# Kernel optimization log

Measured on AMD Instinct MI355X. Metric: run time of the kernel, lower is better.

## Reference

```python
import jax, jax.numpy as jnp
import numpy as np

B, S, E, H, ROT, MAXP = 2, 1024, 2048, 16, 64, 2048
HD = E // H
EPS = 1e-12  # torch F.normalize default eps


def _sinusoidal_positions(num_pos, dim):
    # GPT-J create_sinusoidal_positions: concat(sin, cos) along feature dim
    inv_freq = 1.0 / (10000.0 ** (np.arange(0, dim, 2, dtype=np.float32) / dim))
    sinusoid = np.einsum("i,j->ij", np.arange(num_pos, dtype=np.float32), inv_freq)
    return jnp.asarray(np.concatenate([np.sin(sinusoid), np.cos(sinusoid)], axis=-1))


def _rotate_every_two(x):
    x1 = x[..., ::2]
    x2 = x[..., 1::2]
    return jnp.stack((-x2, x1), axis=-1).reshape(x.shape)


def _apply_rotary(t, sin, cos):
    # t: [B,S,H,rot]; sin/cos: [B,S,rot/2] -> repeat_interleave(2) -> [B,S,1,rot]
    sin = jnp.repeat(sin, 2, axis=-1)[:, :, None, :]
    cos = jnp.repeat(cos, 2, axis=-1)[:, :, None, :]
    return t * cos + _rotate_every_two(t) * sin


def setup_inputs() -> dict:
    key = jax.random.key(0)
    ks = jax.random.split(key, 5)
    hidden_states = jax.random.normal(ks[0], (B, S, E), dtype=jnp.float32)
    w_q = jax.random.normal(ks[1], (E, E), dtype=jnp.float32) * 0.02
    w_k = jax.random.normal(ks[2], (E, E), dtype=jnp.float32) * 0.02
    w_v = jax.random.normal(ks[3], (E, E), dtype=jnp.float32) * 0.02
    w_o = jax.random.normal(ks[4], (E, E), dtype=jnp.float32) * 0.02
    norm_const = 0.5 * jnp.ones((1, H, 1, 1), dtype=jnp.float32)
    attention_mask = jnp.zeros((B, 1, 1, S), dtype=jnp.float32)  # 0 = attend (HF additive mask)
    position_ids = jnp.tile(jnp.arange(S, dtype=jnp.int32)[None, :], (B, 1))
    return {"hidden_states": hidden_states, "w_q": w_q, "w_k": w_k, "w_v": w_v,
            "w_o": w_o, "norm_const": norm_const, "attention_mask": attention_mask,
            "position_ids": position_ids}


def reference(hidden_states, w_q, w_k, w_v, w_o, norm_const, attention_mask, position_ids):
    b, s, e = hidden_states.shape
    # projections (nn.Linear, no bias): y = x @ W.T
    q = (hidden_states @ w_q.T).reshape(b, s, H, HD)  # rotary layout [B,S,H,hd]
    k = (hidden_states @ w_k.T).reshape(b, s, H, HD)
    v = (hidden_states @ w_v.T).reshape(b, s, H, HD).transpose(0, 2, 1, 3)  # [B,H,S,hd]

    embed = _sinusoidal_positions(MAXP, ROT)          # [MAXP, ROT]
    sincos = embed[position_ids]                      # [B,S,ROT]
    sin, cos = jnp.split(sincos, 2, axis=-1)          # each [B,S,ROT/2]

    # partial rotary on first ROT dims
    q = jnp.concatenate([_apply_rotary(q[..., :ROT], sin, cos), q[..., ROT:]], axis=-1)
    k = jnp.concatenate([_apply_rotary(k[..., :ROT], sin, cos), k[..., ROT:]], axis=-1)
    q = q.transpose(0, 2, 1, 3)  # [B,H,S,hd]
    k = k.transpose(0, 2, 1, 3)

    causal = jnp.tril(jnp.ones((s, s), dtype=bool))[None, None]   # [1,1,S,S]
    mask0 = (attention_mask == 0)                                  # [B,1,1,S] bool

    # value rescale: per-query count of visible keys ** sigmoid(norm_const), clamped >= 1
    counts = jnp.sum(causal & mask0, axis=-1, keepdims=True).astype(jnp.float32)  # [B,1,S,1]
    denom = jnp.maximum(counts ** jax.nn.sigmoid(norm_const), 1.0)                # [B,H,S,1]
    v = v / denom

    # L2-normalize q/k (torch F.normalize: x / max(||x||, eps))
    q = q / jnp.maximum(jnp.linalg.norm(q, axis=-1, keepdims=True), EPS)
    k = k / jnp.maximum(jnp.linalg.norm(k, axis=-1, keepdims=True), EPS)

    mask_t = jnp.swapaxes(mask0, -1, -2)  # [B,1,S,1]
    q = q * mask_t
    k = k * mask_t
    v = v * mask_t

    attn_weights = jnp.einsum("bhqd,bhkd->bhqk", q, k)     # cosine similarities
    attn_weights = jnp.where(causal, attn_weights, 0.0)
    attn_output = jnp.einsum("bhqk,bhkd->bhqd", attn_weights, v)

    attn_output = attn_output.transpose(0, 2, 1, 3).reshape(b, s, e)
    return attn_output @ w_o.T
```

## Files before the change

### kernel.cpp

```cpp
#include <hip/hip_runtime.h>
#include <math.h>

#define B 2
#define S 1024
#define E 2048
#define H 16
#define HD 128
#define ROT 64
#define EPSN 1e-12f

using half8 = __attribute__((ext_vector_type(8))) _Float16;
using half4 = __attribute__((ext_vector_type(4))) _Float16;
using half2 = __attribute__((ext_vector_type(2))) _Float16;
using f32x4 = __attribute__((ext_vector_type(4))) float;

__device__ __forceinline__ void gl_lds16(const void* g, void* l) {
    __builtin_amdgcn_global_load_lds(
        (const __attribute__((address_space(1))) unsigned int*)g,
        (__attribute__((address_space(3))) unsigned int*)l, 16, 0, 0);
}

#define BARX()  asm volatile("s_barrier" ::: "memory")
#define LGKM0() asm volatile("s_waitcnt lgkmcnt(0)" ::: "memory")
#define VMW(n)  asm volatile("s_waitcnt vmcnt(" #n ")" ::: "memory")

__global__ __launch_bounds__(256) void f2h5(const float* __restrict__ x0,
                                            const float* __restrict__ x1,
                                            const float* __restrict__ x2,
                                            const float* __restrict__ x3,
                                            const float* __restrict__ x4,
                                            _Float16* __restrict__ y0,
                                            _Float16* __restrict__ y1,
                                            _Float16* __restrict__ y2,
                                            _Float16* __restrict__ y3,
                                            _Float16* __restrict__ y4) {
    const float* xs[5] = {x0, x1, x2, x3, x4};
    _Float16*    ys[5] = {y0, y1, y2, y3, y4};
    const int t = blockIdx.y;
    const int i = blockIdx.x * 256 + threadIdx.x;
    float4 v = ((const float4*)xs[t])[i];
    half4 h;
    h[0] = (_Float16)v.x; h[1] = (_Float16)v.y;
    h[2] = (_Float16)v.z; h[3] = (_Float16)v.w;
    ((half4*)ys[t])[i] = h;
}

__global__ __launch_bounds__(512, 2) void gemm_qkv256(
        const _Float16* __restrict__ hs,
        const _Float16* __restrict__ wq,
        const _Float16* __restrict__ wk,
        const _Float16* __restrict__ wv,
        _Float16* __restrict__ qo,
        _Float16* __restrict__ ko,
        _Float16* __restrict__ vo) {
    __shared__ uint4 L[8][1024];

    const int lid = (int)blockIdx.x;
    const int swz = (lid & 7) * 24 + (lid >> 3);
    const int z   = swz >> 6;
    const int gm  = (swz & 63) >> 3;
    const int gn  = swz & 7;
    const _Float16* Wp = (z == 0) ? wq : (z == 1) ? wk : wv;
    _Float16*     Cout = (z == 0) ? qo : (z == 1) ? ko : vo;
    const int mBase = gm << 8;
    const int nBase = gn << 8;

    const int tid   = (int)threadIdx.x;
    const int lane  = tid & 63;
    const int w     = tid >> 6;
    const int l15   = lane & 15;
    const int lq    = lane >> 4;
    const int wm4   = (w >> 2) << 2;
    const int wn2   = (w & 3) << 1;
    const int wbase = tid & 448;

    f32x4 acc[2][2][4][2];
#pragma unroll
    for (int X = 0; X < 2; ++X)
#pragma unroll
        for (int Y = 0; Y < 2; ++Y)
#pragma unroll
            for (int mt = 0; mt < 4; ++mt)
#pragma unroll
                for (int nt = 0; nt < 2; ++nt)
                    acc[X][Y][mt][nt] = (f32x4){0.f, 0.f, 0.f, 0.f};

    half8 af[4][2], wf[2][2];

    auto stage = [&](int slot, const _Float16* src, int rowBase, int hf, int kt) {
#pragma unroll
        for (int j = 0; j < 2; ++j) {
            const int c  = (j << 9) + tid;
            const int rb = c >> 7;
            const int q  = (c >> 4) & 7;
            const int r  = c & 15;
            gl_lds16(&src[(size_t)(rowBase + hf * 128 + rb * 16 + r) * E +
                          kt * 64 + q * 8],
                     &L[slot][(j << 9) + wbase]);
        }
    };
    auto ldsA = [&](int db, int X) {
#pragma unroll
        for (int mt = 0; mt < 4; ++mt)
#pragma unroll
            for (int ks = 0; ks < 2; ++ks)
                af[mt][ks] = *(const half8*)&L[db * 2 + X]
                    [(wm4 + mt) * 128 + (ks * 4 + lq) * 16 + l15];
    };
    auto ldsB = [&](int db, int Y) {
#pragma unroll
        for (int nt = 0; nt < 2; ++nt)
#pragma unroll
            for (int ks = 0; ks < 2; ++ks)
                wf[nt][ks] = *(const half8*)&L[4 + db * 2 + Y]
                    [(wn2 + nt) * 128 + (ks * 4 + lq) * 16 + l15];
    };
    auto mma = [&](int X, int Y) {
        __builtin_amdgcn_s_setprio(1);
#pragma unroll
        for (int mt = 0; mt < 4; ++mt)
#pragma unroll
            for (int nt = 0; nt < 2; ++nt)
#pragma unroll
                for (int ks = 0; ks < 2; ++ks)
                    acc[X][Y][mt][nt] = __builtin_amdgcn_mfma_f32_16x16x32_f16(
                        af[mt][ks], wf[nt][ks], acc[X][Y][mt][nt], 0, 0, 0);
        __builtin_amdgcn_s_setprio(0);
    };

    stage(0, hs, mBase, 0, 0);
    stage(4, Wp, nBase, 0, 0);
    stage(1, hs, mBase, 1, 0);
    stage(5, Wp, nBase, 1, 0);
    stage(2, hs, mBase, 0, 1);
    stage(7, Wp, nBase, 1, 1);
    stage(3, hs, mBase, 1, 1);
    VMW(6);
    BARX();

    for (int j = 0; j < 16; ++j) {
        const int tB  = 2 * j + 1;
        const int tN0 = 2 * j + 2;
        const int tN1 = 2 * j + 3;
        const bool more = (j < 15);

        ldsA(0, 0); ldsB(0, 0);
        stage(6, Wp, nBase, 0, tB);
        BARX(); LGKM0();
        mma(0, 0);
        BARX();

        ldsB(0, 1);
        if (more) stage(0, hs, mBase, 0, tN0);
        BARX(); LGKM0();
        mma(0, 1);
        BARX();

        ldsA(0, 1);
        if (more) stage(5, Wp, nBase, 1, tN0);
        BARX(); LGKM0();
        mma(1, 1);
        BARX();

        ldsB(0, 0);
        if (more) { stage(1, hs, mBase, 1, tN0); VMW(4); }
        else      { VMW(0); }
        BARX(); LGKM0();
        mma(1, 0);
        BARX();

        ldsA(1, 0); ldsB(1, 0);
        if (more) stage(4, Wp, nBase, 0, tN0);
        BARX(); LGKM0();
        mma(0, 0);
        BARX();

        ldsB(1, 1);
        if (more) stage(2, hs, mBase, 0, tN1);
        BARX(); LGKM0();
        mma(0, 1);
        BARX();

        ldsA(1, 1);
        if (more) stage(7, Wp, nBase, 1, tN1);
        BARX(); LGKM0();
        mma(1, 1);
        BARX();

        ldsB(1, 0);
        if (more) stage(3, hs, mBase, 1, tN1);
        VMW(4);
        BARX(); LGKM0();
        mma(1, 0);
        BARX();
    }

#pragma unroll
    for (int X = 0; X < 2; ++X)
#pragma unroll
        for (int Y = 0; Y < 2; ++Y)
#pragma unroll
            for (int mt = 0; mt < 4; ++mt)
#pragma unroll
                for (int nt = 0; nt < 2; ++nt)
#pragma unroll
                    for (int r = 0; r < 4; ++r) {
                        int row = mBase + X * 128 + (w >> 2) * 64 + mt * 16 + lq * 4 + r;
                        int col = nBase + Y * 128 + (w & 3) * 32 + nt * 16 + l15;
                        int b = row >> 10, s = row & (S - 1);
                        int h = col >> 7,  d = col & (HD - 1);
                        Cout[(((size_t)b * H + h) * S + s) * HD + d] =
                            (_Float16)acc[X][Y][mt][nt][r];
                    }
}

__global__ __launch_bounds__(256) void gemm_out(const _Float16* __restrict__ A,
                                                const _Float16* __restrict__ Wp,
                                                float* __restrict__ C) {
    __shared__ uint4 As_l[2][512];
    __shared__ uint4 Ws_l[2][512];
    const int lid = (int)blockIdx.x;
    const int swz = (lid & 7) * 32 + (lid >> 3);
    const int gm  = swz >> 4;
    const int gn  = swz & 15;
    const int tid  = threadIdx.x;
    const int lane = tid & 63;
    const int w    = tid >> 6;
    const int wm   = (w >> 1) * 64;
    const int wn   = (w & 1) * 64;
    const int l15  = lane & 15;
    const int lq   = lane >> 4;
    const int r16  = lane & 15;
    const int kq4  = lane >> 4;
    const int mBase = gm * 128;
    const int nBase = gn * 128;

    f32x4 acc[4][4];
#pragma unroll
    for (int mt = 0; mt < 4; ++mt)
#pragma unroll
        for (int nt = 0; nt < 4; ++nt)
            acc[mt][nt] = (f32x4){0.f, 0.f, 0.f, 0.f};

    auto stage = [&](int bf, int k0) {
#pragma unroll
        for (int i = 0; i < 2; ++i) {
            int rb = w * 2 + i;
            gl_lds16(&A[(size_t)(mBase + rb * 16 + r16) * E + k0 + kq4 * 8],
                     &As_l[bf][rb * 64]);
            gl_lds16(&Wp[(size_t)(nBase + rb * 16 + r16) * E + k0 + kq4 * 8],
                     &Ws_l[bf][rb * 64]);
        }
    };

    stage(0, 0);
    const int nIter = E / 32;
    for (int it = 0; it < nIter; ++it) {
        __syncthreads();
        if (it + 1 < nIter) stage((it + 1) & 1, (it + 1) * 32);

        const int cur = it & 1;
        half8 af[4], wfr[4];
#pragma unroll
        for (int t = 0; t < 4; ++t) {
            int rbA = (wm >> 4) + t;
            int rbW = (wn >> 4) + t;
            af[t]  = *(const half8*)&As_l[cur][rbA * 64 + lq * 16 + l15];
            wfr[t] = *(const half8*)&Ws_l[cur][rbW * 64 + lq * 16 + l15];
        }
#pragma unroll
        for (int mt = 0; mt < 4; ++mt)
#pragma unroll
            for (int nt = 0; nt < 4; ++nt)
                acc[mt][nt] = __builtin_amdgcn_mfma_f32_16x16x32_f16(
                    af[mt], wfr[nt], acc[mt][nt], 0, 0, 0);
    }

#pragma unroll
    for (int mt = 0; mt < 4; ++mt)
#pragma unroll
        for (int nt = 0; nt < 4; ++nt)
#pragma unroll
            for (int r = 0; r < 4; ++r) {
                int row = mBase + wm + mt * 16 + lq * 4 + r;
                int col = nBase + wn + nt * 16 + l15;
                C[(size_t)row * E + col] = acc[mt][nt][r];
            }
}

__global__ __launch_bounds__(256) void rotary_norm(_Float16* __restrict__ qh,
                                                   _Float16* __restrict__ kh,
                                                   const float* __restrict__ am,
                                                   const int* __restrict__ pos) {
    const int wave = threadIdx.x >> 6;
    const int lane = threadIdx.x & 63;
    const int item = blockIdx.x * 4 + wave;
    const int b = item / (H * S);
    const int h = (item / S) % H;
    const int s = item % S;

    const float p = (float)pos[b * S + s];
    float co = 1.f, si = 0.f;
    if (lane < 32) {
        float ang = p * expf(-0.28782313662425574f * (float)lane);
        sincosf(ang, &si, &co);
    }
    const float valid = (am[b * S + s] == 0.f) ? 1.f : 0.f;
    const size_t base = ((size_t)(b * H + h) * S + s) * HD;

    _Float16* bufs[2] = {qh, kh};
#pragma unroll
    for (int a = 0; a < 2; ++a) {
        _Float16* ptr = bufs[a];
        half2 xin = *(const half2*)&ptr[base + 2 * lane];
        float x0 = (float)xin[0], x1 = (float)xin[1];
        float y0, y1;
        if (lane < 32) {
            y0 = x0 * co - x1 * si;
            y1 = x1 * co + x0 * si;
        } else {
            y0 = x0;
            y1 = x1;
        }
        float ss = y0 * y0 + y1 * y1;
#pragma unroll
        for (int off = 32; off > 0; off >>= 1)
            ss += __shfl_xor(ss, off);
        float scale = valid / fmaxf(sqrtf(ss), EPSN);
        half2 xo;
        xo[0] = (_Float16)(y0 * scale);
        xo[1] = (_Float16)(y1 * scale);
        *(half2*)&ptr[base + 2 * lane] = xo;
    }
}

__global__ __launch_bounds__(256) void vprep(const _Float16* __restrict__ v,
                                             _Float16* __restrict__ vt,
                                             const float* __restrict__ am,
                                             const float* __restrict__ nc) {
    __shared__ _Float16 T[HD][72];
    __shared__ float sscale[64];
    const int bh = blockIdx.y;
    const int b = bh >> 4, h = bh & 15;
    const int s0 = blockIdx.x * 64;
    const int tid = threadIdx.x;

    if (tid < 64) {
        const int lane = tid;
        float basec = 0.f;
        for (int j0 = 0; j0 < s0; j0 += 64) {
            float z = (am[b * S + j0 + lane] == 0.f) ? 1.f : 0.f;
#pragma unroll
            for (int off = 32; off > 0; off >>= 1)
                z += __shfl_xor(z, off);
            basec += z;
        }
        float zown = (am[b * S + s0 + lane] == 0.f) ? 1.f : 0.f;
        float sc = zown;
#pragma unroll
        for (int off = 1; off < 64; off <<= 1) {
            float u = __shfl_up(sc, off);
            if (lane >= off) sc += u;
        }
        float cntv = basec + sc;
        float sig = 1.f / (1.f + expf(-nc[h]));
        float denom = fmaxf(powf(cntv, sig), 1.f);
        sscale[lane] = zown / denom;
    }
    __syncthreads();

#pragma unroll
    for (int j = 0; j < 4; ++j) {
        int f = tid + j * 256;
        int s = f >> 4, c8 = f & 15;
        half8 x = *(const half8*)&v[((size_t)bh * S + s0 + s) * HD + c8 * 8];
        float sc = sscale[s];
#pragma unroll
        for (int i = 0; i < 8; ++i)
            T[c8 * 8 + i][s] = (_Float16)((float)x[i] * sc);
    }
    __syncthreads();

#pragma unroll
    for (int j = 0; j < 4; ++j) {
        int f = tid + j * 256;
        int d = f >> 3, c8 = f & 7;
        *(uint4*)&vt[((size_t)bh * HD + d) * S + s0 + c8 * 8] =
            *(const uint4*)&T[d][c8 * 8];
    }
}

__global__ __launch_bounds__(256) void attn_mfma(const _Float16* __restrict__ qh,
                                                 const _Float16* __restrict__ kh,
                                                 const _Float16* __restrict__ vt,
                                                 _Float16* __restrict__ o) {
    __shared__ _Float16 Ks[64][136];
    __shared__ _Float16 Vs[HD][72];
    __shared__ _Float16 Ps[64][72];

    const int qt = (int)gridDim.x - 1 - (int)blockIdx.x;
    const int bh = blockIdx.y;
    const int b = bh >> 4, h = bh & 15;
    const int tid = threadIdx.x;
    const int lane = tid & 63;
    const int w = tid >> 6;
    const int l15 = lane & 15;
    const int lq = lane >> 4;
    const int qBase = qt * 64;
    const size_t sd_base = (size_t)bh * S * HD;

    half8 qf[4];
#pragma unroll
    for (int ks = 0; ks < 4; ++ks)
        qf[ks] = *(const half8*)&qh[sd_base + (size_t)(qBase + w * 16 + l15) * HD +
                                    ks * 32 + lq * 8];

    f32x4 oacc[8];
#pragma unroll
    for (int dt = 0; dt < 8; ++dt)
        oacc[dt] = (f32x4){0.f, 0.f, 0.f, 0.f};

    const int nkc = qt + 1;
    uint4 pk[4], pv[4];
#pragma unroll
    for (int j = 0; j < 4; ++j) {
        int f = tid + j * 256;
        int rK = f >> 4, c8K = f & 15;
        int rV = f >> 3, c8V = f & 7;
        pk[j] = *(const uint4*)&kh[sd_base + (size_t)rK * HD + c8K * 8];
        pv[j] = *(const uint4*)&vt[sd_base + (size_t)rV * S + c8V * 8];
    }

    for (int kc = 0; kc < nkc; ++kc) {
        __syncthreads();
#pragma unroll
        for (int j = 0; j < 4; ++j) {
            int f = tid + j * 256;
            int rK = f >> 4, c8K = f & 15;
            int rV = f >> 3, c8V = f & 7;
            *(uint4*)&Ks[rK][c8K * 8] = pk[j];
            *(uint4*)&Vs[rV][c8V * 8] = pv[j];
        }
        __syncthreads();

        if (kc + 1 < nkc) {
            const int kB = (kc + 1) * 64;
#pragma unroll
            for (int j = 0; j < 4; ++j) {
                int f = tid + j * 256;
                int rK = f >> 4, c8K = f & 15;
                int rV = f >> 3, c8V = f & 7;
                pk[j] = *(const uint4*)&kh[sd_base + (size_t)(kB + rK) * HD + c8K * 8];
                pv[j] = *(const uint4*)&vt[sd_base + (size_t)rV * S + kB + c8V * 8];
            }
        }

        const int kBase = kc * 64;
        f32x4 sacc[4];
#pragma unroll
        for (int nt = 0; nt < 4; ++nt)
            sacc[nt] = (f32x4){0.f, 0.f, 0.f, 0.f};
#pragma unroll
        for (int nt = 0; nt < 4; ++nt)
#pragma unroll
            for (int ks = 0; ks < 4; ++ks) {
                half8 kf = *(const half8*)&Ks[nt * 16 + l15][ks * 32 + lq * 8];
                sacc[nt] = __builtin_amdgcn_mfma_f32_16x16x32_f16(qf[ks], kf,
                                                                  sacc[nt], 0, 0, 0);
            }

#pragma unroll
        for (int nt = 0; nt < 4; ++nt)
#pragma unroll
            for (int r = 0; r < 4; ++r) {
                int qg = qBase + w * 16 + lq * 4 + r;
                int kg = kBase + nt * 16 + l15;
                float sv = (kg <= qg) ? sacc[nt][r] : 0.f;
                Ps[w * 16 + lq * 4 + r][nt * 16 + l15] = (_Float16)sv;
            }

        half8 pf[2];
        pf[0] = *(const half8*)&Ps[w * 16 + l15][lq * 8];
        pf[1] = *(const half8*)&Ps[w * 16 + l15][32 + lq * 8];
#pragma unroll
        for (int dt = 0; dt < 8; ++dt)
#pragma unroll
            for (int ks = 0; ks < 2; ++ks) {
                half8 vf = *(const half8*)&Vs[dt * 16 + l15][ks * 32 + lq * 8];
                oacc[dt] = __builtin_amdgcn_mfma_f32_16x16x32_f16(pf[ks], vf,
                                                                  oacc[dt], 0, 0, 0);
            }
    }

#pragma unroll
    for (int dt = 0; dt < 8; ++dt)
#pragma unroll
        for (int r = 0; r < 4; ++r) {
            size_t off = (size_t)(b * S + qBase + w * 16 + lq * 4 + r) * E +
                         h * HD + dt * 16 + l15;
            o[off] = (_Float16)oacc[dt][r];
        }
}

extern "C" void kernel_launch(void* const* d_in, const int* in_sizes, int n_in,
                              void* d_out, int out_size, void* d_ws, size_t ws_size,
                              hipStream_t stream) {
    (void)in_sizes; (void)n_in; (void)out_size; (void)ws_size;
    const float* hs = (const float*)d_in[0];
    const float* wq = (const float*)d_in[1];
    const float* wk = (const float*)d_in[2];
    const float* wv = (const float*)d_in[3];
    const float* wo = (const float*)d_in[4];
    const float* nc = (const float*)d_in[5];
    const float* am = (const float*)d_in[6];
    const int*  pos = (const int*)d_in[7];
    float* out = (float*)d_out;

    const size_t act = (size_t)B * S * E;
    _Float16* hsb = (_Float16*)d_ws;
    _Float16* wqb = hsb + act;
    _Float16* wkb = wqb + act;
    _Float16* wvb = wkb + act;
    _Float16* wob = wvb + act;
    _Float16* qhh = wob + act;
    _Float16* khh = qhh + act;
    _Float16* vhh = khh + act;
    _Float16* vtt = vhh + act;
    _Float16* abb = vtt + act;

    f2h5<<<dim3((int)(act / 4 / 256), 5), 256, 0, stream>>>(
        hs, wq, wk, wv, wo, hsb, wqb, wkb, wvb, wob);

    gemm_qkv256<<<192, 512, 0, stream>>>(hsb, wqb, wkb, wvb, qhh, khh, vhh);

    rotary_norm<<<(B * H * S) / 4, 256, 0, stream>>>(qhh, khh, am, pos);
    vprep<<<dim3(S / 64, B * H), 256, 0, stream>>>(vhh, vtt, am, nc);

    attn_mfma<<<dim3(S / 64, B * H), 256, 0, stream>>>(qhh, khh, vtt, abb);

    gemm_out<<<256, 256, 0, stream>>>(abb, wob, out);
}
```

Before: 357.3 us.

## Replace quadratic causal attention with chunked linear attention using prefix K^T V states

The attention has no softmax, so causal attention can be computed as a linear recurrence. The new code forms per-chunk K^T V outer products in fp16, prefix-sums them across 16 chunks, and has each query tile combine Q times its prefix state with an intra-chunk masked local attention. This removes the serial loop over all earlier key chunks in the attention kernel. In exchange it adds a K transpose, two extra kernels, a 16 MB intermediate written and read in workspace aliased onto the freed weight buffers, and fp16 rounding of accumulated states.

```diff
diff --git a/kernel.cpp b/kernel.cpp
--- a/kernel.cpp
+++ b/kernel.cpp
@@ -335,7 +335,9 @@
 }
 
 __global__ __launch_bounds__(256) void vprep(const _Float16* __restrict__ v,
+                                             const _Float16* __restrict__ k,
                                              _Float16* __restrict__ vt,
+                                             _Float16* __restrict__ kt,
                                              const float* __restrict__ am,
                                              const float* __restrict__ nc) {
     __shared__ _Float16 T[HD][72];
@@ -380,7 +382,6 @@
             T[c8 * 8 + i][s] = (_Float16)((float)x[i] * sc);
     }
     __syncthreads();
-
 #pragma unroll
     for (int j = 0; j < 4; ++j) {
         int f = tid + j * 256;
@@ -388,17 +389,134 @@
         *(uint4*)&vt[((size_t)bh * HD + d) * S + s0 + c8 * 8] =
             *(const uint4*)&T[d][c8 * 8];
     }
-}
-
-__global__ __launch_bounds__(256) void attn_mfma(const _Float16* __restrict__ qh,
-                                                 const _Float16* __restrict__ kh,
-                                                 const _Float16* __restrict__ vt,
-                                                 _Float16* __restrict__ o) {
+
+    __syncthreads();
+#pragma unroll
+    for (int j = 0; j < 4; ++j) {
+        int f = tid + j * 256;
+        int s = f >> 4, c8 = f & 15;
+        half8 x = *(const half8*)&k[((size_t)bh * S + s0 + s) * HD + c8 * 8];
+#pragma unroll
+        for (int i = 0; i < 8; ++i)
+            T[c8 * 8 + i][s] = x[i];
+    }
+    __syncthreads();
+#pragma unroll
+    for (int j = 0; j < 4; ++j) {
+        int f = tid + j * 256;
+        int d = f >> 3, c8 = f & 7;
+        *(uint4*)&kt[((size_t)bh * HD + d) * S + s0 + c8 * 8] =
+            *(const uint4*)&T[d][c8 * 8];
+    }
+}
+
+__global__ __launch_bounds__(256) void kvouter(const _Float16* __restrict__ kt,
+                                               const _Float16* __restrict__ vt,
+                                               _Float16* __restrict__ ut) {
+    __shared__ __align__(16) _Float16 SB[2 * 128 * 72];
+    _Float16 (*Kt_s)[72] = (_Float16(*)[72])SB;
+    _Float16 (*Vt_s)[72] = (_Float16(*)[72])(SB + 128 * 72);
+    const int c  = blockIdx.x;
+    const int bh = blockIdx.y;
+    const int tid = threadIdx.x;
+    const int lane = tid & 63, w = tid >> 6;
+    const int l15 = lane & 15, lq = lane >> 4;
+    const size_t ds_b = (size_t)bh * HD * S + (size_t)c * 64;
+
+    uint4 pk[4], pv[4];
+#pragma unroll
+    for (int j = 0; j < 4; ++j) {
+        int f = tid + j * 256;
+        int d = f >> 3, c8 = f & 7;
+        pk[j] = *(const uint4*)&kt[ds_b + (size_t)d * S + c8 * 8];
+        pv[j] = *(const uint4*)&vt[ds_b + (size_t)d * S + c8 * 8];
+    }
+#pragma unroll
+    for (int j = 0; j < 4; ++j) {
+        int f = tid + j * 256;
+        int d = f >> 3, c8 = f & 7;
+        *(uint4*)&Kt_s[d][c8 * 8] = pk[j];
+        *(uint4*)&Vt_s[d][c8 * 8] = pv[j];
+    }
+    __syncthreads();
+
+    f32x4 acc[2][8];
+#pragma unroll
+    for (int mt = 0; mt < 2; ++mt)
+#pragma unroll
+        for (int nt = 0; nt < 8; ++nt)
+            acc[mt][nt] = (f32x4){0.f, 0.f, 0.f, 0.f};
+
+#pragma unroll
+    for (int ks = 0; ks < 2; ++ks) {
+        half8 af[2], wf[8];
+#pragma unroll
+        for (int mt = 0; mt < 2; ++mt)
+            af[mt] = *(const half8*)&Kt_s[(w * 2 + mt) * 16 + l15][ks * 32 + lq * 8];
+#pragma unroll
+        for (int nt = 0; nt < 8; ++nt)
+            wf[nt] = *(const half8*)&Vt_s[nt * 16 + l15][ks * 32 + lq * 8];
+#pragma unroll
+        for (int mt = 0; mt < 2; ++mt)
+#pragma unroll
+            for (int nt = 0; nt < 8; ++nt)
+                acc[mt][nt] = __builtin_amdgcn_mfma_f32_16x16x32_f16(
+                    af[mt], wf[nt], acc[mt][nt], 0, 0, 0);
+    }
+    __syncthreads();
+
+    _Float16* Mb = SB;
+#pragma unroll
+    for (int mt = 0; mt < 2; ++mt)
+#pragma unroll
+        for (int nt = 0; nt < 8; ++nt)
+#pragma unroll
+            for (int r = 0; r < 4; ++r) {
+                int dk = (w * 2 + mt) * 16 + lq * 4 + r;
+                int flat = nt * 2048 + (dk >> 5) * 512 +
+                           (l15 + ((dk >> 3) & 3) * 16) * 8 + (dk & 7);
+                Mb[flat] = (_Float16)acc[mt][nt][r];
+            }
+    __syncthreads();
+
+    const size_t ub = ((size_t)bh * 16 + c) << 14;
+#pragma unroll
+    for (int j = 0; j < 8; ++j) {
+        int f = tid + j * 256;
+        *(uint4*)&ut[ub + (size_t)f * 8] = *(const uint4*)&Mb[f * 8];
+    }
+}
+
+__global__ __launch_bounds__(256) void prefix16(_Float16* __restrict__ u) {
+    const int sl = blockIdx.x & 7;
+    const int bh = blockIdx.x >> 3;
+    const size_t base = (size_t)bh * 16 * 16384 + sl * 2048 + threadIdx.x * 8;
+    float acc[8] = {0.f, 0.f, 0.f, 0.f, 0.f, 0.f, 0.f, 0.f};
+    half8 nxt = *(const half8*)&u[base];
+#pragma unroll
+    for (int c = 0; c < 16; ++c) {
+        half8 cur = nxt;
+        if (c < 15) nxt = *(const half8*)&u[base + (size_t)(c + 1) * 16384];
+        half8 outv;
+#pragma unroll
+        for (int i = 0; i < 8; ++i) outv[i] = (_Float16)acc[i];
+        *(half8*)&u[base + (size_t)c * 16384] = outv;
+#pragma unroll
+        for (int i = 0; i < 8; ++i) acc[i] += (float)cur[i];
+    }
+}
+
+__global__ __launch_bounds__(256) void attn_local(const _Float16* __restrict__ qh,
+                                                  const _Float16* __restrict__ kh,
+                                                  const _Float16* __restrict__ vt,
+                                                  const _Float16* __restrict__ mt,
+                                                  _Float16* __restrict__ o) {
     __shared__ _Float16 Ks[64][136];
     __shared__ _Float16 Vs[HD][72];
     __shared__ _Float16 Ps[64][72];
-
-    const int qt = (int)gridDim.x - 1 - (int)blockIdx.x;
+    __shared__ uint4 Ms[2048];
+
+    const int qt = blockIdx.x;
     const int bh = blockIdx.y;
     const int b = bh >> 4, h = bh & 15;
     const int tid = threadIdx.x;
@@ -415,91 +533,93 @@
         qf[ks] = *(const half8*)&qh[sd_base + (size_t)(qBase + w * 16 + l15) * HD +
                                     ks * 32 + lq * 8];
 
+    const _Float16* mtc = mt + (((size_t)bh * 16 + qt) << 14);
+#pragma unroll
+    for (int rr = 0; rr < 8; ++rr)
+        gl_lds16(&mtc[(size_t)((rr * 4 + w) * 64 + lane) * 8],
+                 &Ms[(rr * 4 + w) * 64]);
+
+    uint4 pk[4], pv[4];
+#pragma unroll
+    for (int j = 0; j < 4; ++j) {
+        int f = tid + j * 256;
+        int rK = f >> 4, c8K = f & 15;
+        int rV = f >> 3, c8V = f & 7;
+        pk[j] = *(const uint4*)&kh[sd_base + (size_t)(qBase + rK) * HD + c8K * 8];
+        pv[j] = *(const uint4*)&vt[sd_base + (size_t)rV * S + qBase + c8V * 8];
+    }
+#pragma unroll
+    for (int j = 0; j < 4; ++j) {
+        int f = tid + j * 256;
+        int rK = f >> 4, c8K = f & 15;
+        int rV = f >> 3, c8V = f & 7;
+        *(uint4*)&Ks[rK][c8K * 8] = pk[j];
+        *(uint4*)&Vs[rV][c8V * 8] = pv[j];
+    }
+    __syncthreads();
+
+    f32x4 sacc[4];
+#pragma unroll
+    for (int nt = 0; nt < 4; ++nt)
+        sacc[nt] = (f32x4){0.f, 0.f, 0.f, 0.f};
+#pragma unroll
+    for (int nt = 0; nt < 4; ++nt)
+#pragma unroll
+        for (int ks = 0; ks < 4; ++ks) {
+            half8 kf = *(const half8*)&Ks[nt * 16 + l15][ks * 32 + lq * 8];
+            sacc[nt] = __builtin_amdgcn_mfma_f32_16x16x32_f16(qf[ks], kf,
+                                                              sacc[nt], 0, 0, 0);
+        }
+
+#pragma unroll
+    for (int nt = 0; nt < 4; ++nt)
+#pragma unroll
+        for (int r = 0; r < 4; ++r) {
+            int ql = w * 16 + lq * 4 + r;
+            int kl = nt * 16 + l15;
+            float sv = (kl <= ql) ? sacc[nt][r] : 0.f;
+            Ps[ql][kl] = (_Float16)sv;
+        }
+
     f32x4 oacc[8];
 #pragma unroll
     for (int dt = 0; dt < 8; ++dt)
         oacc[dt] = (f32x4){0.f, 0.f, 0.f, 0.f};
-
-    const int nkc = qt + 1;
-    uint4 pk[4], pv[4];
-#pragma unroll
-    for (int j = 0; j < 4; ++j) {
-        int f = tid + j * 256;
-        int rK = f >> 4, c8K = f & 15;
-        int rV = f >> 3, c8V = f & 7;
-        pk[j] = *(const uint4*)&kh[sd_base + (size_t)rK * HD + c8K * 8];
-        pv[j] = *(const uint4*)&vt[sd_base + (size_t)rV * S + c8V * 8];
-    }
-
-    for (int kc = 0; kc < nkc; ++kc) {
-        __syncthreads();
-#pragma unroll
-        for (int j = 0; j < 4; ++j) {
-            int f = tid + j * 256;
-            int rK = f >> 4, c8K = f & 15;
-            int rV = f >> 3, c8V = f & 7;
-            *(uint4*)&Ks[rK][c8K * 8] = pk[j];
-            *(uint4*)&Vs[rV][c8V * 8] = pv[j];
-        }
-        __syncthreads();
-
-        if (kc + 1 < nkc) {
-            const int kB = (kc + 1) * 64;
-#pragma unroll
-            for (int j = 0; j < 4; ++j) {
-                int f = tid + j * 256;
-                int rK = f >> 4, c8K = f & 15;
-                int rV = f >> 3, c8V = f & 7;
-                pk[j] = *(const uint4*)&kh[sd_base + (size_t)(kB + rK) * HD + c8K * 8];
-                pv[j] = *(const uint4*)&vt[sd_base + (size_t)rV * S + kB + c8V * 8];
-            }
-        }
-
-        const int kBase = kc * 64;
-        f32x4 sacc[4];
-#pragma unroll
-        for (int nt = 0; nt < 4; ++nt)
-            sacc[nt] = (f32x4){0.f, 0.f, 0.f, 0.f};
-#pragma unroll
-        for (int nt = 0; nt < 4; ++nt)
-#pragma unroll
-            for (int ks = 0; ks < 4; ++ks) {
-                half8 kf = *(const half8*)&Ks[nt * 16 + l15][ks * 32 + lq * 8];
-                sacc[nt] = __builtin_amdgcn_mfma_f32_16x16x32_f16(qf[ks], kf,
-                                                                  sacc[nt], 0, 0, 0);
-            }
-
-#pragma unroll
-        for (int nt = 0; nt < 4; ++nt)
-#pragma unroll
-            for (int r = 0; r < 4; ++r) {
-                int qg = qBase + w * 16 + lq * 4 + r;
-                int kg = kBase + nt * 16 + l15;
-                float sv = (kg <= qg) ? sacc[nt][r] : 0.f;
-                Ps[w * 16 + lq * 4 + r][nt * 16 + l15] = (_Float16)sv;
-            }
-
-        half8 pf[2];
-        pf[0] = *(const half8*)&Ps[w * 16 + l15][lq * 8];
-        pf[1] = *(const half8*)&Ps[w * 16 + l15][32 + lq * 8];
-#pragma unroll
-        for (int dt = 0; dt < 8; ++dt)
-#pragma unroll
-            for (int ks = 0; ks < 2; ++ks) {
-                half8 vf = *(const half8*)&Vs[dt * 16 + l15][ks * 32 + lq * 8];
-                oacc[dt] = __builtin_amdgcn_mfma_f32_16x16x32_f16(pf[ks], vf,
-                                                                  oacc[dt], 0, 0, 0);
-            }
-    }
-
 #pragma unroll
     for (int dt = 0; dt < 8; ++dt)
 #pragma unroll
-        for (int r = 0; r < 4; ++r) {
-            size_t off = (size_t)(b * S + qBase + w * 16 + lq * 4 + r) * E +
-                         h * HD + dt * 16 + l15;
-            o[off] = (_Float16)oacc[dt][r];
-        }
+        for (int km = 0; km < 4; ++km) {
+            half8 mf = *(const half8*)&Ms[(dt * 4 + km) * 64 + lane];
+            oacc[dt] = __builtin_amdgcn_mfma_f32_16x16x32_f16(qf[km], mf,
+                                                              oacc[dt], 0, 0, 0);
+        }
+    __syncthreads();
+
+    half8 pf[2];
+    pf[0] = *(const half8*)&Ps[w * 16 + l15][lq * 8];
+    pf[1] = *(const half8*)&Ps[w * 16 + l15][32 + lq * 8];
+#pragma unroll
+    for (int dt = 0; dt < 8; ++dt)
+#pragma unroll
+        for (int ks = 0; ks < 2; ++ks) {
+            half8 vf = *(const half8*)&Vs[dt * 16 + l15][ks * 32 + lq * 8];
+            oacc[dt] = __builtin_amdgcn_mfma_f32_16x16x32_f16(pf[ks], vf,
+                                                              oacc[dt], 0, 0, 0);
+        }
+
+#pragma unroll
+    for (int dt = 0; dt < 8; ++dt)
+#pragma unroll
+        for (int r = 0; r < 4; ++r)
+            Ks[w * 16 + lq * 4 + r][dt * 16 + l15] = (_Float16)oacc[dt][r];
+    __syncthreads();
+#pragma unroll
+    for (int j = 0; j < 4; ++j) {
+        int f = tid + j * 256;
+        int ql = f >> 4, c8 = f & 15;
+        *(uint4*)&o[(size_t)(b * S + qBase + ql) * E + h * HD + c8 * 8] =
+            *(const uint4*)&Ks[ql][c8 * 8];
+    }
 }
 
 extern "C" void kernel_launch(void* const* d_in, const int* in_sizes, int n_in,
@@ -527,6 +647,8 @@
     _Float16* vhh = khh + act;
     _Float16* vtt = vhh + act;
     _Float16* abb = vtt + act;
+    _Float16* ktt = hsb;
+    _Float16* utm = wqb;
 
     f2h5<<<dim3((int)(act / 4 / 256), 5), 256, 0, stream>>>(
         hs, wq, wk, wv, wo, hsb, wqb, wkb, wvb, wob);
@@ -534,9 +656,11 @@
     gemm_qkv256<<<192, 512, 0, stream>>>(hsb, wqb, wkb, wvb, qhh, khh, vhh);
 
     rotary_norm<<<(B * H * S) / 4, 256, 0, stream>>>(qhh, khh, am, pos);
-    vprep<<<dim3(S / 64, B * H), 256, 0, stream>>>(vhh, vtt, am, nc);
-
-    attn_mfma<<<dim3(S / 64, B * H), 256, 0, stream>>>(qhh, khh, vtt, abb);
+    vprep<<<dim3(S / 64, B * H), 256, 0, stream>>>(vhh, khh, vtt, ktt, am, nc);
+
+    kvouter<<<dim3(16, B * H), 256, 0, stream>>>(ktt, vtt, utm);
+    prefix16<<<B * H * 8, 256, 0, stream>>>(utm);
+    attn_local<<<dim3(16, B * H), 256, 0, stream>>>(qhh, khh, vtt, utm, abb);
 
     gemm_out<<<256, 256, 0, stream>>>(abb, wob, out);
 }
```

New measurement: 301.4 us. 1.19x faster.
